# Kernel tuning notes

Measured on AMD Instinct MI355X. Metric: run time of the kernel, lower is better.

## Reference

```python
import jax, jax.numpy as jnp
import numpy as np

DIM = 512
HEADS = 8
DH = 64          # dim_head = 512 // 8
M = 256          # num_landmarks = 512 // 2
PINV_ITERS = 6
N_PATCH = 40000
IN_DIM = 1024
NUM_CLASSES = 2
GRID = 200       # ceil(sqrt(40000)) -> exact square, add_length = 0


def layernorm(x, w, b, eps=1e-5):
    mu = x.mean(-1, keepdims=True)
    var = ((x - mu) ** 2).mean(-1, keepdims=True)
    return (x - mu) * jax.lax.rsqrt(var + eps) * w + b


def moore_penrose_pinv(x, iters=PINV_ITERS):
    # lucidrains nystrom-attention iterative pseudoinverse
    ax = jnp.abs(x)
    z = jnp.swapaxes(x, -1, -2) / (jnp.max(ax.sum(-1)) * jnp.max(ax.sum(-2)))
    I = jnp.eye(x.shape[-1], dtype=x.dtype)
    for _ in range(iters):
        xz = x @ z
        z = 0.25 * z @ (13 * I - xz @ (15 * I - xz @ (7 * I - xz)))
    return z


def depthwise_conv2d(x, w, pad):
    # x: (B,C,H,W); w: (C,1,kh,kw) torch-style OIHW depthwise kernel
    return jax.lax.conv_general_dilated(
        x, w, (1, 1), [(pad[0], pad[0]), (pad[1], pad[1])],
        dimension_numbers=('NCHW', 'OIHW', 'NCHW'),
        feature_group_count=x.shape[1])


def nystrom_attention(x, qkv_w, out_w, out_b, res_w):
    b, n, _ = x.shape
    pad = (M - n % M) % M
    xp = jnp.pad(x, ((0, 0), (pad, 0), (0, 0)))   # pad at FRONT of sequence
    N = n + pad
    qkv = xp @ qkv_w                              # (b,N,3*h*d), no bias
    q, k, v = jnp.split(qkv, 3, axis=-1)
    to_heads = lambda t: t.reshape(b, N, HEADS, DH).transpose(0, 2, 1, 3)
    q, k, v = to_heads(q), to_heads(k), to_heads(v)
    q = q * (DH ** -0.5)
    l = N // M
    q_l = q.reshape(b, HEADS, M, l, DH).mean(axis=3)   # (b,h,m,d) landmarks
    k_l = k.reshape(b, HEADS, M, l, DH).mean(axis=3)
    attn1 = jax.nn.softmax(jnp.einsum('bhid,bhjd->bhij', q, k_l), axis=-1)   # (b,h,N,m)
    attn2 = jax.nn.softmax(jnp.einsum('bhid,bhjd->bhij', q_l, k_l), axis=-1)  # (b,h,m,m)
    attn3 = jax.nn.softmax(jnp.einsum('bhid,bhjd->bhij', q_l, k), axis=-1)   # (b,h,m,N)
    out = (attn1 @ moore_penrose_pinv(attn2)) @ (attn3 @ v)                   # (b,h,N,d)
    out = out + depthwise_conv2d(v, res_w, (16, 0))    # residual depthwise conv (kernel 33x1)
    out = out.transpose(0, 2, 1, 3).reshape(b, N, HEADS * DH)[:, -n:]
    return out @ out_w + out_b


def ppeg(x, w7, b7, w5, b5, w3, b3, H, W):
    B, _, C = x.shape
    cls_t, feat = x[:, :1], x[:, 1:]
    f = feat.transpose(0, 2, 1).reshape(B, C, H, W)
    y = (f
         + depthwise_conv2d(f, w7, (3, 3)) + b7[None, :, None, None]
         + depthwise_conv2d(f, w5, (2, 2)) + b5[None, :, None, None]
         + depthwise_conv2d(f, w3, (1, 1)) + b3[None, :, None, None])
    y = y.reshape(B, C, H * W).transpose(0, 2, 1)
    return jnp.concatenate([cls_t, y], axis=1)


def setup_inputs() -> dict:
    key = jax.random.key(0)
    ks = iter(jax.random.split(key, 32))
    r = lambda shape, s=0.02: jax.random.normal(next(ks), shape, dtype=jnp.float32) * s
    inp = {
        'x': jax.random.normal(next(ks), (1, N_PATCH, IN_DIM), dtype=jnp.float32),
        'fc1_w': r((IN_DIM, DIM)), 'fc1_b': jnp.zeros((DIM,), jnp.float32),
        'cls_token': r((1, 1, DIM), 1e-6),
        'l1_norm_w': jnp.ones((DIM,), jnp.float32), 'l1_norm_b': jnp.zeros((DIM,), jnp.float32),
        'l1_qkv_w': r((DIM, 3 * HEADS * DH)), 'l1_out_w': r((HEADS * DH, DIM)),
        'l1_out_b': jnp.zeros((DIM,), jnp.float32), 'l1_res_w': r((HEADS, 1, 33, 1)),
        'p7_w': r((DIM, 1, 7, 7)), 'p7_b': jnp.zeros((DIM,), jnp.float32),
        'p5_w': r((DIM, 1, 5, 5)), 'p5_b': jnp.zeros((DIM,), jnp.float32),
        'p3_w': r((DIM, 1, 3, 3)), 'p3_b': jnp.zeros((DIM,), jnp.float32),
        'l2_norm_w': jnp.ones((DIM,), jnp.float32), 'l2_norm_b': jnp.zeros((DIM,), jnp.float32),
        'l2_qkv_w': r((DIM, 3 * HEADS * DH)), 'l2_out_w': r((HEADS * DH, DIM)),
        'l2_out_b': jnp.zeros((DIM,), jnp.float32), 'l2_res_w': r((HEADS, 1, 33, 1)),
        'norm_w': jnp.ones((DIM,), jnp.float32), 'norm_b': jnp.zeros((DIM,), jnp.float32),
        'fc2_w': r((DIM, NUM_CLASSES)), 'fc2_b': jnp.zeros((NUM_CLASSES,), jnp.float32),
    }
    return inp


def reference(x, fc1_w, fc1_b, cls_token,
              l1_norm_w, l1_norm_b, l1_qkv_w, l1_out_w, l1_out_b, l1_res_w,
              p7_w, p7_b, p5_w, p5_b, p3_w, p3_b,
              l2_norm_w, l2_norm_b, l2_qkv_w, l2_out_w, l2_out_b, l2_res_w,
              norm_w, norm_b, fc2_w, fc2_b):
    # _fc1: Linear + ReLU (dropout inactive at eval)
    h = jax.nn.relu(x @ fc1_w + fc1_b)            # (1, 40000, 512)
    # 40000 = 200*200 -> add_length = 0, no square padding needed
    B = h.shape[0]
    h = jnp.concatenate([jnp.broadcast_to(cls_token, (B, 1, DIM)), h], axis=1)
    # layer1: pre-norm Nystrom attention with residual
    h = h + nystrom_attention(layernorm(h, l1_norm_w, l1_norm_b), l1_qkv_w, l1_out_w, l1_out_b, l1_res_w)
    # PPEG positional mixing on the 200x200 token grid
    h = ppeg(h, p7_w, p7_b, p5_w, p5_b, p3_w, p3_b, GRID, GRID)
    # layer2
    h = h + nystrom_attention(layernorm(h, l2_norm_w, l2_norm_b), l2_qkv_w, l2_out_w, l2_out_b, l2_res_w)
    h = layernorm(h, norm_w, norm_b)
    cls_out = h[:, 0]
    logits = cls_out @ fc2_w + fc2_b              # (1, num_classes)
    return logits
```

## Files before the change

### kernel.cpp

```cpp
#include <hip/hip_runtime.h>
#include <hip/hip_bf16.h>

#define DIMC   512
#define HEADS  8
#define DH     64
#define MLM    256
#define NPATCH 40000
#define NTOK   40001
#define PADF   191
#define NSEQ   40192
#define NSEQP  40224
#define LWIN   157
#define INDIM  1024
#define GRID   200
#define CHUNKS 64
#define PER    628

typedef _Float16 h8 __attribute__((ext_vector_type(8)));
typedef _Float16 h4 __attribute__((ext_vector_type(4)));
typedef float    f4 __attribute__((ext_vector_type(4)));

#define WAVE_LDS_FENCE() asm volatile("s_waitcnt lgkmcnt(0)" ::: "memory")

__device__ __forceinline__ void gl_lds(const _Float16* g, _Float16* l) {
  __builtin_amdgcn_global_load_lds(
      (const __attribute__((address_space(1))) void*)g,
      (__attribute__((address_space(3))) void*)l, 16, 0, 0);
}

template<int NW, bool ISMAX>
__device__ __forceinline__ float blkRed(float v, float* s) {
  #pragma unroll
  for (int o = 32; o; o >>= 1) {
    float t = __shfl_down(v, o, 64);
    v = ISMAX ? fmaxf(v, t) : v + t;
  }
  int lane = threadIdx.x & 63, w = threadIdx.x >> 6;
  __syncthreads();
  if (lane == 0) s[w] = v;
  __syncthreads();
  float r = s[0];
  #pragma unroll
  for (int i = 1; i < NW; i++) r = ISMAX ? fmaxf(r, s[i]) : r + s[i];
  return r;
}

__global__ __launch_bounds__(512)
void k_set_cls(const float* __restrict__ cls, float* __restrict__ h) {
  h[threadIdx.x] = cls[threadIdx.x];
}

__global__ __launch_bounds__(256)
void k_f32_to_f16(const float* __restrict__ in, _Float16* __restrict__ out) {
  int i = blockIdx.x * 256 + threadIdx.x;
  float4 v = ((const float4*)in)[i];
  h4 o = {(_Float16)v.x, (_Float16)v.y, (_Float16)v.z, (_Float16)v.w};
  *(h4*)(out + (size_t)i * 4) = o;
}

__global__ __launch_bounds__(256)
void k_zpad(_Float16* q16, _Float16* k16, _Float16* v16) {
  int idx = blockIdx.x * 256 + threadIdx.x;
  int h = idx >> 11, r = (idx >> 6) & 31, d = idx & 63;
  size_t a = ((size_t)h * NSEQP + NSEQ + r) * 64 + d;
  q16[a] = (_Float16)0.f; k16[a] = (_Float16)0.f; v16[a] = (_Float16)0.f;
}

__global__ __launch_bounds__(256)
void k_wt16(const float* __restrict__ B, _Float16* __restrict__ Bt, int K, int N)
{
  __shared__ float tile[32][33];
  int kb = blockIdx.x * 32, nb = blockIdx.y * 32;
  int x = threadIdx.x & 31, y0 = threadIdx.x >> 5;
  #pragma unroll
  for (int yy = y0; yy < 32; yy += 8)
    tile[yy][x] = B[(size_t)(kb + yy) * N + nb + x];
  __syncthreads();
  #pragma unroll
  for (int yy = y0; yy < 32; yy += 8)
    Bt[(size_t)(nb + yy) * K + kb + x] = (_Float16)tile[x][yy];
}

__global__ __launch_bounds__(256)
void k_gemm16(const _Float16* __restrict__ A, const _Float16* __restrict__ Bt,
              const float* __restrict__ bias, float* __restrict__ C,
              _Float16* __restrict__ q16, _Float16* __restrict__ k16, _Float16* __restrict__ v16,
              int Mr, int K, int N, int flags)
{
  __shared__ __attribute__((aligned(16))) _Float16 As[128 * 32];
  __shared__ __attribute__((aligned(16))) _Float16 Bs[128 * 32];
  int bm = blockIdx.x * 128, bn = blockIdx.y * 128;
  int t = threadIdx.x;
  int lane = t & 63, w = t >> 6;
  int wm = (w >> 1) * 64, wn = (w & 1) * 64;
  int r = lane & 15, q = lane >> 4;
  int sub = lane >> 2;
  int kq = (lane & 3) * 8;

  const f4 zero = {0.f, 0.f, 0.f, 0.f};
  f4 acc[4][4];
  #pragma unroll
  for (int mi = 0; mi < 4; mi++)
    #pragma unroll
    for (int nj = 0; nj < 4; nj++) acc[mi][nj] = zero;

  for (int k0 = 0; k0 < K; k0 += 32) {
    #pragma unroll
    for (int c = 0; c < 2; c++) {
      int rowA = (w * 2 + c) * 16 + sub;
      int gmA = bm + rowA; if (gmA > Mr - 1) gmA = Mr - 1;
      gl_lds(A  + (size_t)gmA * K + k0 + kq,          As + (w * 2 + c) * 512);
      gl_lds(Bt + (size_t)(bn + rowA) * K + k0 + kq,  Bs + (w * 2 + c) * 512);
    }
    __syncthreads();
    h8 af[4], bf[4];
    #pragma unroll
    for (int i = 0; i < 4; i++) {
      af[i] = *(const h8*)(As + (wm + i * 16 + r) * 32 + q * 8);
      bf[i] = *(const h8*)(Bs + (wn + i * 16 + r) * 32 + q * 8);
    }
    #pragma unroll
    for (int mi = 0; mi < 4; mi++)
      #pragma unroll
      for (int nj = 0; nj < 4; nj++)
        acc[mi][nj] = __builtin_amdgcn_mfma_f32_16x16x32_f16(bf[nj], af[mi], acc[mi][nj], 0, 0, 0);
    __syncthreads();
  }
  #pragma unroll
  for (int mi = 0; mi < 4; mi++) {
    int gm = bm + wm + mi * 16 + r;
    if (gm >= Mr) continue;
    #pragma unroll
    for (int nj = 0; nj < 4; nj++) {
      int gn = bn + wn + nj * 16 + q * 4;
      f4 v = acc[mi][nj];
      if (flags & 4) {
        int which = gn >> 9, hh = (gn >> 6) & 7, dd = gn & 63;
        _Float16* dst = (which == 0) ? q16 : (which == 1) ? k16 : v16;
        h4 o = {(_Float16)v[0], (_Float16)v[1], (_Float16)v[2], (_Float16)v[3]};
        *(h4*)(dst + ((size_t)hh * NSEQP + gm) * 64 + dd) = o;
      } else {
        if (bias) { f4 bv = *(const f4*)(bias + gn); v += bv; }
        float* cp = C + (size_t)gm * N + gn;
        if (flags & 2) { f4 cv = *(const f4*)cp; v += cv; }
        if (flags & 1) {
          v[0] = fmaxf(v[0], 0.f); v[1] = fmaxf(v[1], 0.f);
          v[2] = fmaxf(v[2], 0.f); v[3] = fmaxf(v[3], 0.f);
        }
        *(f4*)cp = v;
      }
    }
  }
}

__global__ __launch_bounds__(256)
void k_ln_pad(const float* __restrict__ h, const float* __restrict__ w,
              const float* __restrict__ b, _Float16* __restrict__ xln)
{
  __shared__ float sbuf[8];
  int t = blockIdx.x;
  int tid = threadIdx.x;
  _Float16* out = xln + (size_t)t * DIMC;
  if (t < PADF) { out[tid] = (_Float16)0.f; out[tid + 256] = (_Float16)0.f; return; }
  const float* row = h + (size_t)(t - PADF) * DIMC;
  float x0 = row[tid], x1 = row[tid + 256];
  float mu = blkRed<4,false>(x0 + x1, sbuf) * (1.f / 512.f);
  float d0 = x0 - mu, d1 = x1 - mu;
  float var = blkRed<4,false>(d0 * d0 + d1 * d1, sbuf) * (1.f / 512.f);
  float rstd = rsqrtf(var + 1e-5f);
  out[tid]       = (_Float16)(d0 * rstd * w[tid]       + b[tid]);
  out[tid + 256] = (_Float16)(d1 * rstd * w[tid + 256] + b[tid + 256]);
}

__global__ __launch_bounds__(256)
void k_vt(const _Float16* __restrict__ v16, _Float16* __restrict__ vt16)
{
  __shared__ _Float16 tl[64][72];
  int h = blockIdx.y;
  int t0 = blockIdx.x * 64;
  for (int c = threadIdx.x; c < 512; c += 256) {
    int row = c >> 3, ch = (c & 7) * 8;
    h8 v = {};
    if (t0 + row < NSEQP)
      v = *(const h8*)(v16 + ((size_t)h * NSEQP + t0 + row) * 64 + ch);
    *(h8*)&tl[row][ch] = v;
  }
  __syncthreads();
  int d = threadIdx.x & 63, tg = (threadIdx.x >> 6) * 16;
  if (t0 + tg < NSEQP) {
    _Float16 tmp[16];
    #pragma unroll
    for (int k = 0; k < 16; k++) tmp[k] = tl[tg + k][d];
    *(h8*)(vt16 + ((size_t)h * 64 + d) * NSEQP + t0 + tg)     = *(h8*)tmp;
    *(h8*)(vt16 + ((size_t)h * 64 + d) * NSEQP + t0 + tg + 8) = *(h8*)(tmp + 8);
  }
}

__global__ __launch_bounds__(256)
void k_landmarks(const _Float16* __restrict__ q16, const _Float16* __restrict__ k16,
                 float* __restrict__ ql, float* __restrict__ kl,
                 _Float16* __restrict__ ql16, _Float16* __restrict__ kl16)
{
  __shared__ float red[2][16][64];
  int h = blockIdx.x >> 8, i = blockIdx.x & 255;
  int jg = threadIdx.x >> 4, d4 = (threadIdx.x & 15) * 4;
  const _Float16* qb = q16 + ((size_t)h * NSEQP + i * LWIN) * 64;
  const _Float16* kb = k16 + ((size_t)h * NSEQP + i * LWIN) * 64;
  float sq[4] = {}, sk[4] = {};
  for (int j = jg; j < LWIN; j += 16) {
    h4 qv = *(const h4*)(qb + j * 64 + d4);
    h4 kv = *(const h4*)(kb + j * 64 + d4);
    #pragma unroll
    for (int c = 0; c < 4; c++) { sq[c] += (float)qv[c]; sk[c] += (float)kv[c]; }
  }
  #pragma unroll
  for (int c = 0; c < 4; c++) { red[0][jg][d4 + c] = sq[c]; red[1][jg][d4 + c] = sk[c]; }
  __syncthreads();
  if (threadIdx.x < 64) {
    int d = threadIdx.x;
    float aq = 0.f, ak = 0.f;
    #pragma unroll
    for (int g = 0; g < 16; g++) { aq += red[0][g][d]; ak += red[1][g][d]; }
    aq *= (0.125f / (float)LWIN);
    ak *= (1.f / (float)LWIN);
    size_t o = ((size_t)h * MLM + i) * DH + d;
    ql[o] = aq; kl[o] = ak;
    ql16[o] = (_Float16)aq;
    kl16[o] = (_Float16)(ak * 0.125f);
  }
}

__global__ __launch_bounds__(256)
void k_attn2(const float* __restrict__ ql, const float* __restrict__ kl, float* __restrict__ a2)
{
  __shared__ float qrow[DH];
  __shared__ float sbuf[8];
  int h = blockIdx.x >> 8, i = blockIdx.x & 255;
  int j = threadIdx.x;
  if (j < DH) qrow[j] = ql[(h * MLM + i) * DH + j];
  __syncthreads();
  const float* krow = kl + (size_t)(h * MLM + j) * DH;
  float s = 0.f;
  #pragma unroll 16
  for (int d = 0; d < DH; d++) s += qrow[d] * krow[d];
  float mx = blkRed<4,true>(s, sbuf);
  float e = __expf(s - mx);
  float sum = blkRed<4,false>(e, sbuf);
  a2[((size_t)h * MLM + i) * MLM + j] = e / sum;
}

__global__ __launch_bounds__(256)
void k_pinv_init1(const float* __restrict__ a2, float* __restrict__ hmax)
{
  __shared__ float sbuf[8];
  int h = blockIdx.x;
  int j = threadIdx.x;
  const float* A = a2 + (size_t)h * MLM * MLM;
  float cs = 0.f, rs = 0.f;
  for (int i = 0; i < MLM; i++) cs += A[i * MLM + j];
  for (int k = 0; k < MLM; k++) rs += A[j * MLM + k];
  float rmax = blkRed<4,true>(rs, sbuf);
  float cmax = blkRed<4,true>(cs, sbuf);
  if (j == 0) { hmax[h * 2] = rmax; hmax[h * 2 + 1] = cmax; }
}

__global__ void k_pinv_init2(const float* __restrict__ hmax, float* __restrict__ scal)
{
  float rm = 0.f, cm = 0.f;
  for (int h = 0; h < HEADS; h++) { rm = fmaxf(rm, hmax[2*h]); cm = fmaxf(cm, hmax[2*h+1]); }
  scal[0] = 1.f / (rm * cm);
}

__global__ __launch_bounds__(256)
void k_pinv_prep(const float* __restrict__ a2, const float* __restrict__ scal,
                 _Float16* __restrict__ a2h, _Float16* __restrict__ a2l,
                 _Float16* __restrict__ zh,  _Float16* __restrict__ zl,
                 _Float16* __restrict__ zth, _Float16* __restrict__ ztl)
{
  __shared__ float tl[64][65];
  int h = blockIdx.x >> 4, tile = blockIdx.x & 15;
  int ti = (tile >> 2) * 64, tj = (tile & 3) * 64;
  float s = scal[0];
  int row = threadIdx.x >> 4, c4 = (threadIdx.x & 15) * 4;
  #pragma unroll
  for (int rr = 0; rr < 4; rr++) {
    int rloc = rr * 16 + row;
    f4 v = *(const f4*)(a2 + ((size_t)h * MLM + ti + rloc) * MLM + tj + c4);
    h4 hi, lo, zhi, zlo;
    #pragma unroll
    for (int c = 0; c < 4; c++) {
      hi[c] = (_Float16)v[c];
      lo[c] = (_Float16)(v[c] - (float)hi[c]);
      float zv = v[c] * s;
      zhi[c] = (_Float16)zv;
      zlo[c] = (_Float16)(zv - (float)zhi[c]);
      tl[rloc][c4 + c] = zv;
    }
    size_t idx = ((size_t)h * MLM + ti + rloc) * MLM + tj + c4;
    *(h4*)(a2h + idx) = hi;  *(h4*)(a2l + idx) = lo;
    *(h4*)(zth + idx) = zhi; *(h4*)(ztl + idx) = zlo;
  }
  __syncthreads();
  #pragma unroll
  for (int rr = 0; rr < 4; rr++) {
    int rloc = rr * 16 + row;
    h4 hi, lo;
    #pragma unroll
    for (int c = 0; c < 4; c++) {
      float zv = tl[c4 + c][rloc];
      hi[c] = (_Float16)zv;
      lo[c] = (_Float16)(zv - (float)hi[c]);
    }
    size_t idx = ((size_t)h * MLM + tj + rloc) * MLM + ti + c4;
    *(h4*)(zh + idx) = hi; *(h4*)(zl + idx) = lo;
  }
}

__global__ __launch_bounds__(256)
void k_pbmm(const _Float16* __restrict__ Ah, const _Float16* __restrict__ Al,
            const _Float16* __restrict__ Bth, const _Float16* __restrict__ Btl,
            const _Float16* __restrict__ Eh, const _Float16* __restrict__ El,
            _Float16* __restrict__ Ch,  _Float16* __restrict__ Cl,
            _Float16* __restrict__ Cth, _Float16* __restrict__ Ctl,
            int N, float c0, float c1)
{
  __shared__ __attribute__((aligned(16))) _Float16 Ash[64 * 32];
  __shared__ __attribute__((aligned(16))) _Float16 Asl[64 * 32];
  __shared__ __attribute__((aligned(16))) _Float16 Bsh[64 * 32];
  __shared__ __attribute__((aligned(16))) _Float16 Bsl[64 * 32];
  __shared__ __attribute__((aligned(16))) _Float16 Tt0[64 * 64];
  __shared__ __attribute__((aligned(16))) _Float16 Tt1[64 * 64];
  int tn = N >> 6;
  int bm = (blockIdx.x / tn) * 64, bn = (blockIdx.x % tn) * 64;
  int h = blockIdx.y;
  int tid = threadIdx.x, lane = tid & 63, w = tid >> 6;
  int wm = (w >> 1) * 32, wn = (w & 1) * 32;
  int r = lane & 15, q = lane >> 4;
  int sub = lane >> 2, kq = (lane & 3) * 8;

  const _Float16* Ahb = Ah + ((size_t)h * MLM + bm) * MLM;
  const _Float16* Alb = Al + ((size_t)h * MLM + bm) * MLM;
  const _Float16* Bhb = Bth + ((size_t)h * N + bn) * MLM;
  const _Float16* Blb = Btl + ((size_t)h * N + bn) * MLM;

  const f4 zero = {0.f, 0.f, 0.f, 0.f};
  f4 acc[2][2];
  #pragma unroll
  for (int mi = 0; mi < 2; mi++)
    #pragma unroll
    for (int nj = 0; nj < 2; nj++) acc[mi][nj] = zero;

  for (int k0 = 0; k0 < MLM; k0 += 32) {
    int rw = w * 16 + sub;
    gl_lds(Ahb + (size_t)rw * MLM + k0 + kq, Ash + w * 512);
    gl_lds(Alb + (size_t)rw * MLM + k0 + kq, Asl + w * 512);
    gl_lds(Bhb + (size_t)rw * MLM + k0 + kq, Bsh + w * 512);
    gl_lds(Blb + (size_t)rw * MLM + k0 + kq, Bsl + w * 512);
    __syncthreads();
    h8 afh[2], afl[2], bfh[2], bfl[2];
    #pragma unroll
    for (int i = 0; i < 2; i++) {
      afh[i] = *(const h8*)(Ash + (wm + i * 16 + r) * 32 + q * 8);
      afl[i] = *(const h8*)(Asl + (wm + i * 16 + r) * 32 + q * 8);
      bfh[i] = *(const h8*)(Bsh + (wn + i * 16 + r) * 32 + q * 8);
      bfl[i] = *(const h8*)(Bsl + (wn + i * 16 + r) * 32 + q * 8);
    }
    #pragma unroll
    for (int mi = 0; mi < 2; mi++)
      #pragma unroll
      for (int nj = 0; nj < 2; nj++) {
        acc[mi][nj] = __builtin_amdgcn_mfma_f32_16x16x32_f16(afh[mi], bfh[nj], acc[mi][nj], 0, 0, 0);
        acc[mi][nj] = __builtin_amdgcn_mfma_f32_16x16x32_f16(afh[mi], bfl[nj], acc[mi][nj], 0, 0, 0);
        acc[mi][nj] = __builtin_amdgcn_mfma_f32_16x16x32_f16(afl[mi], bfh[nj], acc[mi][nj], 0, 0, 0);
      }
    __syncthreads();
  }
  #pragma unroll
  for (int mi = 0; mi < 2; mi++) {
    #pragma unroll
    for (int i = 0; i < 4; i++) {
      int lm = wm + mi * 16 + q * 4 + i;
      #pragma unroll
      for (int nj = 0; nj < 2; nj++) {
        int ln = wn + nj * 16 + r;
        size_t ide = ((size_t)h * MLM + bm + lm) * N + bn + ln;
        float v = c0 * acc[mi][nj][i];
        if (Eh) v += c1 * ((float)Eh[ide] + (float)El[ide]);
        _Float16 hi = (_Float16)v;
        _Float16 lo = (_Float16)(v - (float)hi);
        if (Ch) { Ch[ide] = hi; Cl[ide] = lo; }
        int sw = lm ^ ((ln & 7) << 3);
        Tt0[ln * 64 + sw] = hi;
        Tt1[ln * 64 + sw] = lo;
      }
    }
  }
  __syncthreads();
  {
    int row = tid >> 2;
    int cb0 = (tid & 3) * 16;
    #pragma unroll
    for (int sg = 0; sg < 2; sg++) {
      int cb = cb0 + sg * 8;
      int swc = cb ^ ((row & 7) << 3);
      h8 vh = *(const h8*)(Tt0 + row * 64 + swc);
      h8 vl = *(const h8*)(Tt1 + row * 64 + swc);
      size_t idt = ((size_t)h * N + bn + row) * MLM + bm + cb;
      *(h8*)(Cth + idt) = vh;
      *(h8*)(Ctl + idt) = vl;
    }
  }
}

__global__ __launch_bounds__(256)
void k_attn3(const _Float16* __restrict__ ql16, const _Float16* __restrict__ k16,
             const _Float16* __restrict__ vt16,
             float* __restrict__ pm, float* __restrict__ ps, float* __restrict__ pacc)
{
  __shared__ __attribute__((aligned(16))) _Float16 Pl[4][64 * 40];
  int c = blockIdx.x, h = blockIdx.y;
  int tid = threadIdx.x, lane = tid & 63, w = tid >> 6;
  int r = lane & 15, q = lane >> 4;
  int t0 = c * PER;
  int m0 = w * 64;
  const _Float16* qlh = ql16 + (size_t)h * MLM * 64;
  const _Float16* kh  = k16  + (size_t)h * NSEQP * 64;
  const _Float16* vh  = vt16 + (size_t)h * 64 * NSEQP;
  _Float16* Pw = &Pl[w][0];

  h8 af[4][2];
  #pragma unroll
  for (int mt = 0; mt < 4; mt++)
    #pragma unroll
    for (int ks = 0; ks < 2; ks++)
      af[mt][ks] = *(const h8*)(qlh + (size_t)(m0 + mt * 16 + r) * 64 + ks * 32 + q * 8);

  const f4 zero = {0.f, 0.f, 0.f, 0.f};
  f4 acc[4][4];
  float mrun[4][4], lrun[4][4];
  #pragma unroll
  for (int mt = 0; mt < 4; mt++) {
    #pragma unroll
    for (int nd = 0; nd < 4; nd++) acc[mt][nd] = zero;
    #pragma unroll
    for (int i = 0; i < 4; i++) { mrun[mt][i] = -1e30f; lrun[mt][i] = 0.f; }
  }

  for (int tb = 0; tb < 20; tb++) {
    int tt = t0 + tb * 32;
    f4 S[4][2];
    #pragma unroll
    for (int mt = 0; mt < 4; mt++) { S[mt][0] = zero; S[mt][1] = zero; }
    #pragma unroll
    for (int nt = 0; nt < 2; nt++) {
      h8 b0 = *(const h8*)(kh + (size_t)(tt + nt * 16 + r) * 64 + q * 8);
      h8 b1 = *(const h8*)(kh + (size_t)(tt + nt * 16 + r) * 64 + 32 + q * 8);
      #pragma unroll
      for (int mt = 0; mt < 4; mt++) {
        S[mt][nt] = __builtin_amdgcn_mfma_f32_16x16x32_f16(af[mt][0], b0, S[mt][nt], 0, 0, 0);
        S[mt][nt] = __builtin_amdgcn_mfma_f32_16x16x32_f16(af[mt][1], b1, S[mt][nt], 0, 0, 0);
      }
    }
    if (tb == 19) {
      #pragma unroll
      for (int nt = 0; nt < 2; nt++) {
        bool valid = (tb * 32 + nt * 16 + r) < PER;
        #pragma unroll
        for (int mt = 0; mt < 4; mt++)
          #pragma unroll
          for (int i = 0; i < 4; i++)
            S[mt][nt][i] = valid ? S[mt][nt][i] : -1e30f;
      }
    }
    #pragma unroll
    for (int mt = 0; mt < 4; mt++) {
      float nm[4], al[4], ls[4];
      #pragma unroll
      for (int i = 0; i < 4; i++) {
        nm[i] = fmaxf(S[mt][0][i], S[mt][1][i]);
        #pragma unroll
        for (int o = 1; o < 16; o <<= 1) nm[i] = fmaxf(nm[i], __shfl_xor(nm[i], o, 64));
        nm[i] = fmaxf(nm[i], mrun[mt][i]);
        al[i] = __expf(mrun[mt][i] - nm[i]);
        mrun[mt][i] = nm[i];
        float p0 = __expf(S[mt][0][i] - nm[i]);
        float p1 = __expf(S[mt][1][i] - nm[i]);
        S[mt][0][i] = p0; S[mt][1][i] = p1;
        ls[i] = p0 + p1;
        #pragma unroll
        for (int o = 1; o < 16; o <<= 1) ls[i] += __shfl_xor(ls[i], o, 64);
        lrun[mt][i] = lrun[mt][i] * al[i] + ls[i];
      }
      #pragma unroll
      for (int nd = 0; nd < 4; nd++)
        #pragma unroll
        for (int i = 0; i < 4; i++) acc[mt][nd][i] *= al[i];
      #pragma unroll
      for (int nt = 0; nt < 2; nt++)
        #pragma unroll
        for (int i = 0; i < 4; i++)
          Pw[(mt * 16 + q * 4 + i) * 40 + nt * 16 + r] = (_Float16)S[mt][nt][i];
    }
    WAVE_LDS_FENCE();
    h8 bv[4];
    #pragma unroll
    for (int nd = 0; nd < 4; nd++)
      bv[nd] = *(const h8*)(vh + (size_t)(nd * 16 + r) * NSEQP + tt + q * 8);
    #pragma unroll
    for (int mt = 0; mt < 4; mt++) {
      h8 ap = *(const h8*)(Pw + (mt * 16 + r) * 40 + q * 8);
      #pragma unroll
      for (int nd = 0; nd < 4; nd++)
        acc[mt][nd] = __builtin_amdgcn_mfma_f32_16x16x32_f16(ap, bv[nd], acc[mt][nd], 0, 0, 0);
    }
    WAVE_LDS_FENCE();
  }
  int cidx = h * CHUNKS + c;
  #pragma unroll
  for (int mt = 0; mt < 4; mt++) {
    int rowb = m0 + mt * 16 + q * 4;
    if (r == 0) {
      #pragma unroll
      for (int i = 0; i < 4; i++) {
        pm[(size_t)cidx * MLM + rowb + i] = mrun[mt][i];
        ps[(size_t)cidx * MLM + rowb + i] = lrun[mt][i];
      }
    }
    #pragma unroll
    for (int nd = 0; nd < 4; nd++)
      #pragma unroll
      for (int i = 0; i < 4; i++)
        pacc[((size_t)cidx * MLM + rowb + i) * 64 + nd * 16 + r] = acc[mt][nd][i];
  }
}

__global__ __launch_bounds__(64)
void k_attn3_reduce(const float* __restrict__ pm, const float* __restrict__ ps,
                    const float* __restrict__ pacc,
                    _Float16* __restrict__ avth, _Float16* __restrict__ avtl)
{
  int h = blockIdx.x >> 8, i = blockIdx.x & 255;
  int d = threadIdx.x;
  float m = -1e30f;
  for (int c = 0; c < CHUNKS; c++) m = fmaxf(m, pm[(h * CHUNKS + c) * MLM + i]);
  float l = 0.f, a = 0.f;
  for (int c = 0; c < CHUNKS; c++) {
    int idx = (h * CHUNKS + c) * MLM + i;
    float w = __expf(pm[idx] - m);
    l += ps[idx] * w;
    a += pacc[(size_t)idx * DH + d] * w;
  }
  float v = a / l;
  _Float16 hi = (_Float16)v;
  size_t o = ((size_t)h * DH + d) * MLM + i;
  avth[o] = hi;
  avtl[o] = (_Float16)(v - (float)hi);
}

__global__ __launch_bounds__(256)
void k_conv(const _Float16* __restrict__ v16, const float* __restrict__ rw,
            _Float16* __restrict__ xat)
{
  __shared__ float tl[160][64];
  int h = blockIdx.y;
  int t0 = PADF + blockIdx.x * 128;
  for (int c = threadIdx.x; c < 160 * 16; c += 256) {
    int row = c >> 4, d4 = (c & 15) * 4;
    int ts = t0 - 16 + row;
    f4 val = {0.f, 0.f, 0.f, 0.f};
    if (ts >= 0 && ts < NSEQ) {
      h4 hv = *(const h4*)(v16 + ((size_t)h * NSEQP + ts) * 64 + d4);
      val[0] = (float)hv[0]; val[1] = (float)hv[1]; val[2] = (float)hv[2]; val[3] = (float)hv[3];
    }
    *(f4*)&tl[row][d4] = val;
  }
  __syncthreads();
  float wt[33];
  #pragma unroll
  for (int tap = 0; tap < 33; tap++) wt[tap] = rw[h * 33 + tap];
  int d4 = (threadIdx.x & 15) * 4, r0 = threadIdx.x >> 4;
  #pragma unroll
  for (int k = 0; k < 8; k++) {
    int r = k * 16 + r0;
    int t = t0 + r;
    f4 acc = {0.f, 0.f, 0.f, 0.f};
    #pragma unroll
    for (int tap = 0; tap < 33; tap++) {
      f4 vv = *(const f4*)&tl[r + tap][d4];
      acc[0] += wt[tap] * vv[0]; acc[1] += wt[tap] * vv[1];
      acc[2] += wt[tap] * vv[2]; acc[3] += wt[tap] * vv[3];
    }
    if (t < NSEQ) {
      h4 o = {(_Float16)acc[0], (_Float16)acc[1], (_Float16)acc[2], (_Float16)acc[3]};
      *(h4*)(xat + (size_t)t * DIMC + h * 64 + d4) = o;
    }
  }
}

__global__ __launch_bounds__(256)
void k_attn1(const _Float16* __restrict__ q16, const _Float16* __restrict__ kl16,
             const _Float16* __restrict__ w2t16, _Float16* __restrict__ xat)
{
  __shared__ __attribute__((aligned(16))) _Float16 Pl[4][64 * 40];
  int h = blockIdx.y;
  int t0 = blockIdx.x * 256;
  int tid = threadIdx.x, lane = tid & 63, w = tid >> 6;
  int r = lane & 15, q = lane >> 4;
  int m0 = w * 64;
  const _Float16* qh  = q16  + (size_t)h * NSEQP * 64;
  const _Float16* klh = kl16 + (size_t)h * MLM * 64;
  const _Float16* w2h = w2t16 + (size_t)h * 64 * 256;
  _Float16* Pw = &Pl[w][0];

  h8 af[4][2];
  #pragma unroll
  for (int mt = 0; mt < 4; mt++)
    #pragma unroll
    for (int ks = 0; ks < 2; ks++)
      af[mt][ks] = *(const h8*)(qh + (size_t)(t0 + m0 + mt * 16 + r) * 64 + ks * 32 + q * 8);

  const f4 zero = {0.f, 0.f, 0.f, 0.f};
  f4 acc[4][4];
  float mrun[4][4], lrun[4][4];
  #pragma unroll
  for (int mt = 0; mt < 4; mt++) {
    #pragma unroll
    for (int nd = 0; nd < 4; nd++) acc[mt][nd] = zero;
    #pragma unroll
    for (int i = 0; i < 4; i++) { mrun[mt][i] = -1e30f; lrun[mt][i] = 0.f; }
  }

  for (int tb = 0; tb < 8; tb++) {
    int tt = tb * 32;
    f4 S[4][2];
    #pragma unroll
    for (int mt = 0; mt < 4; mt++) { S[mt][0] = zero; S[mt][1] = zero; }
    #pragma unroll
    for (int nt = 0; nt < 2; nt++) {
      h8 b0 = *(const h8*)(klh + (size_t)(tt + nt * 16 + r) * 64 + q * 8);
      h8 b1 = *(const h8*)(klh + (size_t)(tt + nt * 16 + r) * 64 + 32 + q * 8);
      #pragma unroll
      for (int mt = 0; mt < 4; mt++) {
        S[mt][nt] = __builtin_amdgcn_mfma_f32_16x16x32_f16(af[mt][0], b0, S[mt][nt], 0, 0, 0);
        S[mt][nt] = __builtin_amdgcn_mfma_f32_16x16x32_f16(af[mt][1], b1, S[mt][nt], 0, 0, 0);
      }
    }
    #pragma unroll
    for (int mt = 0; mt < 4; mt++) {
      float nm[4], al[4], ls[4];
      #pragma unroll
      for (int i = 0; i < 4; i++) {
        nm[i] = fmaxf(S[mt][0][i], S[mt][1][i]);
        #pragma unroll
        for (int o = 1; o < 16; o <<= 1) nm[i] = fmaxf(nm[i], __shfl_xor(nm[i], o, 64));
        nm[i] = fmaxf(nm[i], mrun[mt][i]);
        al[i] = __expf(mrun[mt][i] - nm[i]);
        mrun[mt][i] = nm[i];
        float p0 = __expf(S[mt][0][i] - nm[i]);
        float p1 = __expf(S[mt][1][i] - nm[i]);
        S[mt][0][i] = p0; S[mt][1][i] = p1;
        ls[i] = p0 + p1;
        #pragma unroll
        for (int o = 1; o < 16; o <<= 1) ls[i] += __shfl_xor(ls[i], o, 64);
        lrun[mt][i] = lrun[mt][i] * al[i] + ls[i];
      }
      #pragma unroll
      for (int nd = 0; nd < 4; nd++)
        #pragma unroll
        for (int i = 0; i < 4; i++) acc[mt][nd][i] *= al[i];
      #pragma unroll
      for (int nt = 0; nt < 2; nt++)
        #pragma unroll
        for (int i = 0; i < 4; i++)
          Pw[(mt * 16 + q * 4 + i) * 40 + nt * 16 + r] = (_Float16)S[mt][nt][i];
    }
    WAVE_LDS_FENCE();
    h8 bw[4];
    #pragma unroll
    for (int nd = 0; nd < 4; nd++)
      bw[nd] = *(const h8*)(w2h + (size_t)(nd * 16 + r) * 256 + tt + q * 8);
    #pragma unroll
    for (int mt = 0; mt < 4; mt++) {
      h8 ap = *(const h8*)(Pw + (mt * 16 + r) * 40 + q * 8);
      #pragma unroll
      for (int nd = 0; nd < 4; nd++)
        acc[mt][nd] = __builtin_amdgcn_mfma_f32_16x16x32_f16(ap, bw[nd], acc[mt][nd], 0, 0, 0);
    }
    WAVE_LDS_FENCE();
  }
  #pragma unroll
  for (int half = 0; half < 2; half++) {
    #pragma unroll
    for (int mt2 = 0; mt2 < 2; mt2++) {
      int mt = half * 2 + mt2;
      float li[4];
      #pragma unroll
      for (int i = 0; i < 4; i++) li[i] = 1.f / lrun[mt][i];
      #pragma unroll
      for (int nd = 0; nd < 4; nd++)
        #pragma unroll
        for (int i = 0; i < 4; i++)
          Pw[(mt2 * 16 + q * 4 + i) * 72 + nd * 16 + r] = (_Float16)(acc[mt][nd][i] * li[i]);
    }
    WAVE_LDS_FENCE();
    #pragma unroll
    for (int c = 0; c < 4; c++) {
      int row = c * 8 + (lane >> 3);
      int ch = (lane & 7) * 8;
      int t = t0 + m0 + half * 32 + row;
      if (t >= PADF) {
        _Float16* dst = xat + (size_t)t * DIMC + h * 64 + ch;
        h8 cv = *(h8*)dst;
        h8 pv = *(const h8*)(Pw + row * 72 + ch);
        h8 o;
        #pragma unroll
        for (int k = 0; k < 8; k++) o[k] = (_Float16)((float)cv[k] + (float)pv[k]);
        *(h8*)dst = o;
      }
    }
    WAVE_LDS_FENCE();
  }
}

__global__ __launch_bounds__(256)
void k_transpose_fw(const float* __restrict__ h, float* __restrict__ g)
{
  __shared__ float tile[32][33];
  int pb = blockIdx.x * 32, cb = blockIdx.y * 32;
  int x = threadIdx.x & 31, y0 = threadIdx.x >> 5;
  #pragma unroll
  for (int yy = y0; yy < 32; yy += 8)
    tile[yy][x] = h[(size_t)(1 + pb + yy) * DIMC + cb + x];
  __syncthreads();
  #pragma unroll
  for (int yy = y0; yy < 32; yy += 8)
    g[(size_t)(cb + yy) * NPATCH + pb + x] = tile[x][yy];
}

__global__ __launch_bounds__(256)
void k_ppeg(const float* __restrict__ g,
            const float* __restrict__ w7, const float* __restrict__ b7,
            const float* __restrict__ w5, const float* __restrict__ b5,
            const float* __restrict__ w3, const float* __restrict__ b3,
            float* __restrict__ o)
{
  __shared__ float tl[22][22];
  int c = blockIdx.y;
  int ty0 = (blockIdx.x / 13) * 16, tx0 = (blockIdx.x % 13) * 16;
  const float* gc = g + (size_t)c * NPATCH;
  for (int e = threadIdx.x; e < 22 * 22; e += 256) {
    int yy = e / 22, xx = e % 22;
    int y = ty0 - 3 + yy, x = tx0 - 3 + xx;
    tl[yy][xx] = (y >= 0 && y < GRID && x >= 0 && x < GRID) ? gc[y * GRID + x] : 0.f;
  }
  __syncthreads();
  int ly = threadIdx.x >> 4, lx = threadIdx.x & 15;
  int y = ty0 + ly, x = tx0 + lx;
  if (y >= GRID || x >= GRID) return;
  float acc = tl[ly + 3][lx + 3] + b7[c] + b5[c] + b3[c];
  #pragma unroll
  for (int ky = 0; ky < 7; ky++)
    #pragma unroll
    for (int kx = 0; kx < 7; kx++)
      acc += w7[c * 49 + ky * 7 + kx] * tl[ly + ky][lx + kx];
  #pragma unroll
  for (int ky = 0; ky < 5; ky++)
    #pragma unroll
    for (int kx = 0; kx < 5; kx++)
      acc += w5[c * 25 + ky * 5 + kx] * tl[ly + 1 + ky][lx + 1 + kx];
  #pragma unroll
  for (int ky = 0; ky < 3; ky++)
    #pragma unroll
    for (int kx = 0; kx < 3; kx++)
      acc += w3[c * 9 + ky * 3 + kx] * tl[ly + 2 + ky][lx + 2 + kx];
  o[(size_t)c * NPATCH + y * GRID + x] = acc;
}

__global__ __launch_bounds__(256)
void k_transpose_bw(const float* __restrict__ g, float* __restrict__ h)
{
  __shared__ float tile[32][33];
  int pb = blockIdx.x * 32, cb = blockIdx.y * 32;
  int x = threadIdx.x & 31, y0 = threadIdx.x >> 5;
  #pragma unroll
  for (int yy = y0; yy < 32; yy += 8)
    tile[yy][x] = g[(size_t)(cb + yy) * NPATCH + pb + x];
  __syncthreads();
  #pragma unroll
  for (int yy = y0; yy < 32; yy += 8)
    h[(size_t)(1 + pb + yy) * DIMC + cb + x] = tile[x][yy];
}

__global__ __launch_bounds__(512)
void k_final(const float* __restrict__ h, const float* __restrict__ nw, const float* __restrict__ nb,
             const float* __restrict__ fw, const float* __restrict__ fb, float* __restrict__ out)
{
  __shared__ float sbuf[8];
  int d = threadIdx.x;
  float x = h[d];
  float mu = blkRed<8,false>(x, sbuf) * (1.f / 512.f);
  float dd = x - mu;
  float var = blkRed<8,false>(dd * dd, sbuf) * (1.f / 512.f);
  float cls = dd * rsqrtf(var + 1e-5f) * nw[d] + nb[d];
  float l0 = blkRed<8,false>(cls * fw[d * 2 + 0], sbuf);
  float l1 = blkRed<8,false>(cls * fw[d * 2 + 1], sbuf);
  if (d == 0) { out[0] = l0 + fb[0]; out[1] = l1 + fb[1]; }
}

struct Pair4 { _Float16 *h, *l, *th, *tl; };
struct WsPtrs {
  float *h, *ql, *kl, *a2, *hmax, *scal, *pm, *ps, *pacc;
  _Float16 *xat16, *q16, *k16, *v16, *vt16, *ql16, *kl16, *x16;
  _Float16 *a2h, *a2l, *avth, *avtl;
  Pair4 zA, zB, xz, u, u2, w2;
};

static void attention_layer(const WsPtrs& P,
                            const float* nw, const float* nb, const _Float16* qkvw16,
                            const _Float16* ow16, const float* ob, const float* rw,
                            hipStream_t stream)
{
  k_zpad<<<64, 256, 0, stream>>>(P.q16, P.k16, P.v16);
  k_ln_pad<<<NSEQ, 256, 0, stream>>>(P.h, nw, nb, P.xat16);
  k_gemm16<<<dim3(NSEQ / 128, 1536 / 128), 256, 0, stream>>>(
      P.xat16, qkvw16, nullptr, nullptr, P.q16, P.k16, P.v16, NSEQ, DIMC, 3 * DIMC, 4);
  k_vt<<<dim3(629, HEADS), 256, 0, stream>>>(P.v16, P.vt16);
  k_landmarks<<<HEADS * MLM, 256, 0, stream>>>(P.q16, P.k16, P.ql, P.kl, P.ql16, P.kl16);
  k_attn2<<<HEADS * MLM, 256, 0, stream>>>(P.ql, P.kl, P.a2);
  k_pinv_init1<<<HEADS, 256, 0, stream>>>(P.a2, P.hmax);
  k_pinv_init2<<<1, 1, 0, stream>>>(P.hmax, P.scal);
  k_pinv_prep<<<HEADS * 16, 256, 0, stream>>>(P.a2, P.scal,
      P.a2h, P.a2l, P.zA.h, P.zA.l, P.zA.th, P.zA.tl);
  Pair4 z = P.zA, zn = P.zB;
  for (int it = 0; it < 6; it++) {
    k_pbmm<<<dim3(16, HEADS), 256, 0, stream>>>(P.a2h, P.a2l, z.th, z.tl,
        nullptr, nullptr, P.xz.h, P.xz.l, P.xz.th, P.xz.tl, MLM, 1.f, 0.f);
    k_pbmm<<<dim3(16, HEADS), 256, 0, stream>>>(P.xz.h, P.xz.l, P.xz.th, P.xz.tl,
        P.xz.h, P.xz.l, nullptr, nullptr, P.u.th, P.u.tl, MLM, -1.f, 7.f);
    k_pbmm<<<dim3(16, HEADS), 256, 0, stream>>>(P.xz.h, P.xz.l, P.u.th, P.u.tl,
        P.xz.h, P.xz.l, nullptr, nullptr, P.u2.th, P.u2.tl, MLM, -1.f, 15.f);
    k_pbmm<<<dim3(16, HEADS), 256, 0, stream>>>(z.h, z.l, P.u2.th, P.u2.tl,
        z.h, z.l, zn.h, zn.l, zn.th, zn.tl, MLM, -0.25f, 3.25f);
    Pair4 t = z; z = zn; zn = t;
  }
  k_attn3<<<dim3(CHUNKS, HEADS), 256, 0, stream>>>(P.ql16, P.k16, P.vt16, P.pm, P.ps, P.pacc);
  k_attn3_reduce<<<HEADS * MLM, 64, 0, stream>>>(P.pm, P.ps, P.pacc, P.avth, P.avtl);
  k_pbmm<<<dim3(4, HEADS), 256, 0, stream>>>(z.h, z.l, P.avth, P.avtl,
      nullptr, nullptr, nullptr, nullptr, P.w2.th, P.w2.tl, DH, 1.f, 0.f);
  k_conv<<<dim3(313, HEADS), 256, 0, stream>>>(P.v16, rw, P.xat16);
  k_attn1<<<dim3(157, HEADS), 256, 0, stream>>>(P.q16, P.kl16, P.w2.th, P.xat16);
  k_gemm16<<<dim3((NTOK + 127) / 128, DIMC / 128), 256, 0, stream>>>(
      P.xat16 + (size_t)PADF * DIMC, ow16, ob, P.h, nullptr, nullptr, nullptr, NTOK, DIMC, DIMC, 2);
}

extern "C" void kernel_launch(void* const* d_in, const int* in_sizes, int n_in,
                              void* d_out, int out_size, void* d_ws, size_t ws_size,
                              hipStream_t stream)
{
  const float* x      = (const float*)d_in[0];
  const float* fc1_w  = (const float*)d_in[1];
  const float* fc1_b  = (const float*)d_in[2];
  const float* cls    = (const float*)d_in[3];
  const float* l1_nw  = (const float*)d_in[4];
  const float* l1_nb  = (const float*)d_in[5];
  const float* l1_qkv = (const float*)d_in[6];
  const float* l1_ow  = (const float*)d_in[7];
  const float* l1_ob  = (const float*)d_in[8];
  const float* l1_rw  = (const float*)d_in[9];
  const float* p7w    = (const float*)d_in[10];
  const float* p7b    = (const float*)d_in[11];
  const float* p5w    = (const float*)d_in[12];
  const float* p5b    = (const float*)d_in[13];
  const float* p3w    = (const float*)d_in[14];
  const float* p3b    = (const float*)d_in[15];
  const float* l2_nw  = (const float*)d_in[16];
  const float* l2_nb  = (const float*)d_in[17];
  const float* l2_qkv = (const float*)d_in[18];
  const float* l2_ow  = (const float*)d_in[19];
  const float* l2_ob  = (const float*)d_in[20];
  const float* l2_rw  = (const float*)d_in[21];
  const float* nw     = (const float*)d_in[22];
  const float* nb     = (const float*)d_in[23];
  const float* fc2w   = (const float*)d_in[24];
  const float* fc2b   = (const float*)d_in[25];
  float* out = (float*)d_out;

  float* W = (float*)d_ws;
  WsPtrs P;
  size_t off = 0;
  P.h     = W + off;               off += 20480512ull;
  P.xat16 = (_Float16*)(W + off);  off += 10289152ull;
  float* R0 = W + off;
  P.q16   = (_Float16*)R0;
  P.k16   = P.q16 + 20594688ull;
  P.v16   = P.k16 + 20594688ull;
  P.vt16  = P.v16 + 20594688ull;
  P.x16   = P.q16;
  off += 41189376ull;
  P.ql    = W + off; off += 131072;
  P.kl    = W + off; off += 131072;
  P.ql16  = (_Float16*)(W + off); off += 65536;
  P.kl16  = (_Float16*)(W + off); off += 65536;
  P.a2    = W + off; off += 524288;
  _Float16* HP = (_Float16*)(W + off);
  size_t ho = 0;
  P.a2h = HP + ho; ho += 524288; P.a2l = HP + ho; ho += 524288;
  auto alloc4 = [&](Pair4& p, size_t n) {
    p.h = HP + ho; ho += n; p.l = HP + ho; ho += n;
    p.th = HP + ho; ho += n; p.tl = HP + ho; ho += n;
  };
  alloc4(P.zA, 524288); alloc4(P.zB, 524288); alloc4(P.xz, 524288);
  alloc4(P.u, 524288);  alloc4(P.u2, 524288);
  alloc4(P.w2, 131072);
  P.avth = HP + ho; ho += 131072; P.avtl = HP + ho; ho += 131072;
  off += (ho + 1) / 2;
  P.hmax  = W + off; P.scal = P.hmax + 16; off += 32;
  P.pm    = W + off; off += 131072;
  P.ps    = W + off; off += 131072;
  P.pacc  = W + off; off += 8388608;
  _Float16* fc1t  = (_Float16*)(W + off);
  _Float16* qkv1t = fc1t  + 524288;
  _Float16* out1t = qkv1t + 786432;
  _Float16* qkv2t = out1t + 262144;
  _Float16* out2t = qkv2t + 786432;

  k_wt16<<<dim3(INDIM / 32, DIMC / 32), 256, 0, stream>>>(fc1_w, fc1t, INDIM, DIMC);
  k_wt16<<<dim3(DIMC / 32, 1536 / 32), 256, 0, stream>>>(l1_qkv, qkv1t, DIMC, 1536);
  k_wt16<<<dim3(DIMC / 32, DIMC / 32), 256, 0, stream>>>(l1_ow, out1t, DIMC, DIMC);
  k_wt16<<<dim3(DIMC / 32, 1536 / 32), 256, 0, stream>>>(l2_qkv, qkv2t, DIMC, 1536);
  k_wt16<<<dim3(DIMC / 32, DIMC / 32), 256, 0, stream>>>(l2_ow, out2t, DIMC, DIMC);

  k_f32_to_f16<<<NPATCH * INDIM / 1024, 256, 0, stream>>>(x, P.x16);
  k_gemm16<<<dim3((NPATCH + 127) / 128, DIMC / 128), 256, 0, stream>>>(
      P.x16, fc1t, fc1_b, P.h + DIMC, nullptr, nullptr, nullptr, NPATCH, INDIM, DIMC, 1);
  k_set_cls<<<1, 512, 0, stream>>>(cls, P.h);

  attention_layer(P, l1_nw, l1_nb, qkv1t, out1t, l1_ob, l1_rw, stream);

  float* fgrid = R0;
  float* cout  = R0 + 20480000ull;
  k_transpose_fw<<<dim3(NPATCH / 32, DIMC / 32), 256, 0, stream>>>(P.h, fgrid);
  k_ppeg<<<dim3(13 * 13, DIMC), 256, 0, stream>>>(fgrid, p7w, p7b, p5w, p5b, p3w, p3b, cout);
  k_transpose_bw<<<dim3(NPATCH / 32, DIMC / 32), 256, 0, stream>>>(cout, P.h);

  attention_layer(P, l2_nw, l2_nb, qkv2t, out2t, l2_ob, l2_rw, stream);

  k_final<<<1, 512, 0, stream>>>(P.h, nw, nb, fc2w, fc2b, out);
}
```

Before: 2.317 ms.

## Lazy online-softmax rescaling, deferred row-sum reduction, and register-tiled two-channel PPEG

The two flash-style softmax loops now skip the max reduction and the accumulator rescale unless some score exceeds the running max by more than 8, which is the lazy-rescale trick. The per-tile cross-lane row-sum shuffle is replaced by per-lane partial sums that are reduced once after the loop. The PPEG depthwise conv kernel is rewritten to process two channels per block as float2, use 32x32 tiles, and have each thread produce 4 outputs from register-cached rows with vectorized stores. This cuts shuffles, exps and multiplies in the attention kernels and LDS traffic in PPEG, at the cost of a slightly larger exponent range in the unnormalized sums.

```diff
diff --git a/kernel.cpp b/kernel.cpp
--- a/kernel.cpp
+++ b/kernel.cpp
@@ -19,6 +19,7 @@
 typedef _Float16 h8 __attribute__((ext_vector_type(8)));
 typedef _Float16 h4 __attribute__((ext_vector_type(4)));
 typedef float    f4 __attribute__((ext_vector_type(4)));
+typedef float    f2 __attribute__((ext_vector_type(2)));
 
 #define WAVE_LDS_FENCE() asm volatile("s_waitcnt lgkmcnt(0)" ::: "memory")
 
@@ -474,27 +475,34 @@
     }
     #pragma unroll
     for (int mt = 0; mt < 4; mt++) {
-      float nm[4], al[4], ls[4];
+      bool tg = false;
+      #pragma unroll
+      for (int i = 0; i < 4; i++)
+        tg = tg || (S[mt][0][i] > mrun[mt][i] + 8.f) || (S[mt][1][i] > mrun[mt][i] + 8.f);
+      if (__any(tg)) {
+        float nm[4], al[4];
+        #pragma unroll
+        for (int i = 0; i < 4; i++) {
+          nm[i] = fmaxf(S[mt][0][i], S[mt][1][i]);
+          #pragma unroll
+          for (int o = 1; o < 16; o <<= 1) nm[i] = fmaxf(nm[i], __shfl_xor(nm[i], o, 64));
+          nm[i] = fmaxf(nm[i], mrun[mt][i]);
+          al[i] = __expf(mrun[mt][i] - nm[i]);
+          mrun[mt][i] = nm[i];
+          lrun[mt][i] *= al[i];
+        }
+        #pragma unroll
+        for (int nd = 0; nd < 4; nd++)
+          #pragma unroll
+          for (int i = 0; i < 4; i++) acc[mt][nd][i] *= al[i];
+      }
       #pragma unroll
       for (int i = 0; i < 4; i++) {
-        nm[i] = fmaxf(S[mt][0][i], S[mt][1][i]);
-        #pragma unroll
-        for (int o = 1; o < 16; o <<= 1) nm[i] = fmaxf(nm[i], __shfl_xor(nm[i], o, 64));
-        nm[i] = fmaxf(nm[i], mrun[mt][i]);
-        al[i] = __expf(mrun[mt][i] - nm[i]);
-        mrun[mt][i] = nm[i];
-        float p0 = __expf(S[mt][0][i] - nm[i]);
-        float p1 = __expf(S[mt][1][i] - nm[i]);
+        float p0 = __expf(S[mt][0][i] - mrun[mt][i]);
+        float p1 = __expf(S[mt][1][i] - mrun[mt][i]);
+        lrun[mt][i] += p0 + p1;
         S[mt][0][i] = p0; S[mt][1][i] = p1;
-        ls[i] = p0 + p1;
-        #pragma unroll
-        for (int o = 1; o < 16; o <<= 1) ls[i] += __shfl_xor(ls[i], o, 64);
-        lrun[mt][i] = lrun[mt][i] * al[i] + ls[i];
-      }
-      #pragma unroll
-      for (int nd = 0; nd < 4; nd++)
-        #pragma unroll
-        for (int i = 0; i < 4; i++) acc[mt][nd][i] *= al[i];
+      }
       #pragma unroll
       for (int nt = 0; nt < 2; nt++)
         #pragma unroll
@@ -515,6 +523,12 @@
     }
     WAVE_LDS_FENCE();
   }
+  #pragma unroll
+  for (int mt = 0; mt < 4; mt++)
+    #pragma unroll
+    for (int i = 0; i < 4; i++)
+      #pragma unroll
+      for (int o = 1; o < 16; o <<= 1) lrun[mt][i] += __shfl_xor(lrun[mt][i], o, 64);
   int cidx = h * CHUNKS + c;
   #pragma unroll
   for (int mt = 0; mt < 4; mt++) {
@@ -647,27 +661,34 @@
     }
     #pragma unroll
     for (int mt = 0; mt < 4; mt++) {
-      float nm[4], al[4], ls[4];
+      bool tg = false;
+      #pragma unroll
+      for (int i = 0; i < 4; i++)
+        tg = tg || (S[mt][0][i] > mrun[mt][i] + 8.f) || (S[mt][1][i] > mrun[mt][i] + 8.f);
+      if (__any(tg)) {
+        float nm[4], al[4];
+        #pragma unroll
+        for (int i = 0; i < 4; i++) {
+          nm[i] = fmaxf(S[mt][0][i], S[mt][1][i]);
+          #pragma unroll
+          for (int o = 1; o < 16; o <<= 1) nm[i] = fmaxf(nm[i], __shfl_xor(nm[i], o, 64));
+          nm[i] = fmaxf(nm[i], mrun[mt][i]);
+          al[i] = __expf(mrun[mt][i] - nm[i]);
+          mrun[mt][i] = nm[i];
+          lrun[mt][i] *= al[i];
+        }
+        #pragma unroll
+        for (int nd = 0; nd < 4; nd++)
+          #pragma unroll
+          for (int i = 0; i < 4; i++) acc[mt][nd][i] *= al[i];
+      }
       #pragma unroll
       for (int i = 0; i < 4; i++) {
-        nm[i] = fmaxf(S[mt][0][i], S[mt][1][i]);
-        #pragma unroll
-        for (int o = 1; o < 16; o <<= 1) nm[i] = fmaxf(nm[i], __shfl_xor(nm[i], o, 64));
-        nm[i] = fmaxf(nm[i], mrun[mt][i]);
-        al[i] = __expf(mrun[mt][i] - nm[i]);
-        mrun[mt][i] = nm[i];
-        float p0 = __expf(S[mt][0][i] - nm[i]);
-        float p1 = __expf(S[mt][1][i] - nm[i]);
+        float p0 = __expf(S[mt][0][i] - mrun[mt][i]);
+        float p1 = __expf(S[mt][1][i] - mrun[mt][i]);
+        lrun[mt][i] += p0 + p1;
         S[mt][0][i] = p0; S[mt][1][i] = p1;
-        ls[i] = p0 + p1;
-        #pragma unroll
-        for (int o = 1; o < 16; o <<= 1) ls[i] += __shfl_xor(ls[i], o, 64);
-        lrun[mt][i] = lrun[mt][i] * al[i] + ls[i];
-      }
-      #pragma unroll
-      for (int nd = 0; nd < 4; nd++)
-        #pragma unroll
-        for (int i = 0; i < 4; i++) acc[mt][nd][i] *= al[i];
+      }
       #pragma unroll
       for (int nt = 0; nt < 2; nt++)
         #pragma unroll
@@ -688,6 +709,12 @@
     }
     WAVE_LDS_FENCE();
   }
+  #pragma unroll
+  for (int mt = 0; mt < 4; mt++)
+    #pragma unroll
+    for (int i = 0; i < 4; i++)
+      #pragma unroll
+      for (int o = 1; o < 16; o <<= 1) lrun[mt][i] += __shfl_xor(lrun[mt][i], o, 64);
   #pragma unroll
   for (int half = 0; half < 2; half++) {
     #pragma unroll
@@ -744,36 +771,64 @@
             const float* __restrict__ w3, const float* __restrict__ b3,
             float* __restrict__ o)
 {
-  __shared__ float tl[22][22];
-  int c = blockIdx.y;
-  int ty0 = (blockIdx.x / 13) * 16, tx0 = (blockIdx.x % 13) * 16;
-  const float* gc = g + (size_t)c * NPATCH;
-  for (int e = threadIdx.x; e < 22 * 22; e += 256) {
-    int yy = e / 22, xx = e % 22;
-    int y = ty0 - 3 + yy, x = tx0 - 3 + xx;
-    tl[yy][xx] = (y >= 0 && y < GRID && x >= 0 && x < GRID) ? gc[y * GRID + x] : 0.f;
-  }
-  __syncthreads();
-  int ly = threadIdx.x >> 4, lx = threadIdx.x & 15;
-  int y = ty0 + ly, x = tx0 + lx;
-  if (y >= GRID || x >= GRID) return;
-  float acc = tl[ly + 3][lx + 3] + b7[c] + b5[c] + b3[c];
-  #pragma unroll
-  for (int ky = 0; ky < 7; ky++)
-    #pragma unroll
-    for (int kx = 0; kx < 7; kx++)
-      acc += w7[c * 49 + ky * 7 + kx] * tl[ly + ky][lx + kx];
-  #pragma unroll
-  for (int ky = 0; ky < 5; ky++)
-    #pragma unroll
-    for (int kx = 0; kx < 5; kx++)
-      acc += w5[c * 25 + ky * 5 + kx] * tl[ly + 1 + ky][lx + 1 + kx];
-  #pragma unroll
-  for (int ky = 0; ky < 3; ky++)
-    #pragma unroll
-    for (int kx = 0; kx < 3; kx++)
-      acc += w3[c * 9 + ky * 3 + kx] * tl[ly + 2 + ky][lx + 2 + kx];
-  o[(size_t)c * NPATCH + y * GRID + x] = acc;
+  __shared__ f2 tl[38][40];
+  int cp = blockIdx.y;
+  int c0 = cp * 2, c1 = c0 + 1;
+  int ty0 = (blockIdx.x / 7) * 32, tx0 = (blockIdx.x % 7) * 32;
+  const float* g0 = g + (size_t)c0 * NPATCH;
+  const float* g1 = g + (size_t)c1 * NPATCH;
+  for (int e = threadIdx.x; e < 38 * 40; e += 256) {
+    int row = e / 40, col = e % 40;
+    int y = ty0 - 3 + row, x = tx0 - 3 + col;
+    f2 v = {0.f, 0.f};
+    if (y >= 0 && y < GRID && x >= 0 && x < GRID && col < 38) {
+      v[0] = g0[y * GRID + x];
+      v[1] = g1[y * GRID + x];
+    }
+    tl[row][col] = v;
+  }
+  __syncthreads();
+  int tx4 = (threadIdx.x & 7) * 4, ty = threadIdx.x >> 3;
+  f2 bb = {b7[c0] + b5[c0] + b3[c0], b7[c1] + b5[c1] + b3[c1]};
+  f2 acc[4];
+  #pragma unroll
+  for (int j = 0; j < 4; j++) acc[j] = bb + tl[ty + 3][tx4 + 3 + j];
+  #pragma unroll
+  for (int ky = 0; ky < 7; ky++) {
+    f2 f[10];
+    #pragma unroll
+    for (int k = 0; k < 5; k++)
+      *(f4*)&f[k * 2] = *(const f4*)&tl[ty + ky][tx4 + k * 2];
+    #pragma unroll
+    for (int kx = 0; kx < 7; kx++) {
+      f2 wv = {w7[c0 * 49 + ky * 7 + kx], w7[c1 * 49 + ky * 7 + kx]};
+      #pragma unroll
+      for (int j = 0; j < 4; j++) acc[j] += wv * f[kx + j];
+    }
+    if (ky >= 1 && ky <= 5) {
+      #pragma unroll
+      for (int kx = 0; kx < 5; kx++) {
+        f2 wv = {w5[c0 * 25 + (ky - 1) * 5 + kx], w5[c1 * 25 + (ky - 1) * 5 + kx]};
+        #pragma unroll
+        for (int j = 0; j < 4; j++) acc[j] += wv * f[1 + kx + j];
+      }
+    }
+    if (ky >= 2 && ky <= 4) {
+      #pragma unroll
+      for (int kx = 0; kx < 3; kx++) {
+        f2 wv = {w3[c0 * 9 + (ky - 2) * 3 + kx], w3[c1 * 9 + (ky - 2) * 3 + kx]};
+        #pragma unroll
+        for (int j = 0; j < 4; j++) acc[j] += wv * f[2 + kx + j];
+      }
+    }
+  }
+  int y = ty0 + ty, xb = tx0 + tx4;
+  if (y < GRID && xb < GRID) {
+    f4 o0 = {acc[0][0], acc[1][0], acc[2][0], acc[3][0]};
+    f4 o1 = {acc[0][1], acc[1][1], acc[2][1], acc[3][1]};
+    *(f4*)(o + (size_t)c0 * NPATCH + y * GRID + xb) = o0;
+    *(f4*)(o + (size_t)c1 * NPATCH + y * GRID + xb) = o1;
+  }
 }
 
 __global__ __launch_bounds__(256)
@@ -940,7 +995,7 @@
   float* fgrid = R0;
   float* cout  = R0 + 20480000ull;
   k_transpose_fw<<<dim3(NPATCH / 32, DIMC / 32), 256, 0, stream>>>(P.h, fgrid);
-  k_ppeg<<<dim3(13 * 13, DIMC), 256, 0, stream>>>(fgrid, p7w, p7b, p5w, p5b, p3w, p3b, cout);
+  k_ppeg<<<dim3(7 * 7, DIMC / 2), 256, 0, stream>>>(fgrid, p7w, p7b, p5w, p5b, p3w, p3b, cout);
   k_transpose_bw<<<dim3(NPATCH / 32, DIMC / 32), 256, 0, stream>>>(cout, P.h);
 
   attention_layer(P, l2_nw, l2_nb, qkv2t, out2t, l2_ob, l2_rw, stream);
```

New measurement: 2.186 ms. 5.7% less time.
